# Kernel optimization log

Measured on AMD Instinct MI355X. Metric: run time of the kernel, lower is better.

## Reference

```python
import jax, jax.numpy as jnp
import numpy as np

C = 0.01          # curvature
SQRT_C = C ** 0.5 # 0.1
R = 16            # number of diagonal blocks = out_features / block_size
BS = 256          # block_size
D = R * BS        # 4096


def _artanh(x):
    # Matches torch Artanh: clamp input, grad is 1/(1-xc^2) (straight-through clamp)
    xc = jnp.clip(x, -1.0 + 1e-5, 1.0 - 1e-5)
    xc = x + jax.lax.stop_gradient(xc - x)
    return 0.5 * (jnp.log(1.0 + xc) - jnp.log(1.0 - xc))


def _tanh(x, clamp=15.0):
    return jnp.tanh(jnp.clip(x, -clamp, clamp))


def _norm(x):
    return jnp.linalg.norm(x, axis=-1, keepdims=True)


def _forward(x, weights):
    # expmap0 (poincare ball)
    u_norm = jnp.maximum(_norm(x), 1e-5)
    h = _tanh(SQRT_C * u_norm) * x / (SQRT_C * u_norm)
    # fix_filt = output_hyperbolic.data  -> detach
    h = jax.lax.stop_gradient(h)

    # mobius_matvec with block-diagonal weight; equivalent batched block matmul:
    # mx = h @ block_diag(W_1..W_r).T  ==  per-block h_r @ W_r.T
    xb = h.reshape(h.shape[:-1] + (R, BS))            # [..., r, bs]
    mx = jnp.einsum('...rk,rjk->...rj', xb, weights)  # [..., r, bs]
    mx = mx.reshape(h.shape)

    x_norm = jnp.maximum(_norm(h), 1e-5)
    mx_norm = _norm(mx)
    res_c = _tanh(mx_norm / x_norm * _artanh(SQRT_C * x_norm)) * mx / (mx_norm * SQRT_C)
    cond = jnp.all(mx == 0, axis=-1, keepdims=True)
    res = jnp.where(cond, jnp.zeros((), dtype=res_c.dtype), res_c)

    # _project onto the ball
    nrm = jnp.maximum(_norm(res), 1e-5)
    maxnorm = (1.0 - 1e-3) / SQRT_C
    res = jnp.where(nrm > maxnorm, res / nrm * maxnorm, res)

    # logmap0 (poincare ball)
    y_norm = jnp.maximum(_norm(res), 1e-5)
    return res / y_norm / SQRT_C * _artanh(SQRT_C * y_norm)


def setup_inputs() -> dict:
    key = jax.random.key(0)
    k1, k2 = jax.random.split(key)
    x = jax.random.normal(k1, (4, 2048, D), dtype=jnp.float32)
    # params: init is stack of identity blocks; add small noise so math is non-trivial
    eye = jnp.broadcast_to(jnp.eye(BS, dtype=jnp.float32), (R, BS, BS))
    weights = eye + 0.02 * jax.random.normal(k2, (R, BS, BS), dtype=jnp.float32)
    return {"x": x, "weights": weights}


def reference(x, weights):
    return _forward(x, weights)
```

## Files before the change

### kernel.cpp

```cpp
#include <hip/hip_runtime.h>


typedef __attribute__((ext_vector_type(8))) short short8;
typedef __attribute__((ext_vector_type(4))) float f32x4;

__device__ __forceinline__ ushort f2bf(float f) {
  uint u = __float_as_uint(f);
  return (ushort)((u + 0x7fffu + ((u >> 16) & 1u)) >> 16);
}

__global__ __launch_bounds__(256) void wrepack_kernel(const float* __restrict__ w,
                                                      ushort* __restrict__ wb2) {
  int idx = blockIdx.x * blockDim.x + threadIdx.x;
  int lane = idx & 63;
  int nt = (idx >> 6) & 15;
  int kf = (idx >> 10) & 7;
  int blk = idx >> 13;
  int g = lane >> 4, q = lane & 15;
  const float* src = w + ((size_t)blk << 16) + (size_t)(nt * 16 + q) * 256 + kf * 32 + g * 8;
  float4 v0 = *reinterpret_cast<const float4*>(src);
  float4 v1 = *reinterpret_cast<const float4*>(src + 4);
  ushort o[8] = {f2bf(v0.x), f2bf(v0.y), f2bf(v0.z), f2bf(v0.w),
                 f2bf(v1.x), f2bf(v1.y), f2bf(v1.z), f2bf(v1.w)};
  uint4 p;
  p.x = (uint)o[0] | ((uint)o[1] << 16);
  p.y = (uint)o[2] | ((uint)o[3] << 16);
  p.z = (uint)o[4] | ((uint)o[5] << 16);
  p.w = (uint)o[6] | ((uint)o[7] << 16);
  reinterpret_cast<uint4*>(wb2)[idx] = p;
}

__global__ __launch_bounds__(1024, 4) void hyp_kernel(const float* __restrict__ x,
                                                      const ushort* __restrict__ wb2,
                                                      float* __restrict__ out) {
  __shared__ ushort xs[16 * 4096];
  __shared__ float ssxp[16];
  __shared__ float sspm[16][16];
  __shared__ float gam[16];

  const int tid = threadIdx.x;
  const int w = tid >> 6;
  const int lane = tid & 63;
  const int g = lane >> 4;
  const int q = lane & 15;
  const size_t rowbase = (size_t)blockIdx.x * 16;

  {
    const float4* xr = reinterpret_cast<const float4*>(x + (rowbase + w) * 4096);
    char* xrow = reinterpret_cast<char*>(xs);
    const uint sw = (uint)(w & 7) << 4;
    float ss = 0.f;
#pragma unroll
    for (int chunk = 0; chunk < 16; ++chunk) {
      float4 v = xr[chunk * 64 + lane];
      ss += v.x * v.x + v.y * v.y + v.z * v.z + v.w * v.w;
      uint2 p;
      p.x = (uint)f2bf(v.x) | ((uint)f2bf(v.y) << 16);
      p.y = (uint)f2bf(v.z) | ((uint)f2bf(v.w) << 16);
      uint byte = ((uint)(w * 8192 + (chunk * 64 + lane) * 8)) ^ sw;
      *reinterpret_cast<uint2*>(xrow + byte) = p;
    }
#pragma unroll
    for (int m = 32; m; m >>= 1) ss += __shfl_xor(ss, m, 64);
    if (lane == 0) ssxp[w] = ss;
  }
  __syncthreads();

  f32x4 acc[16];
#pragma unroll
  for (int nt = 0; nt < 16; ++nt) acc[nt] = (f32x4){0.f, 0.f, 0.f, 0.f};

  for (int kf = 0; kf < 8; ++kf) {
    uint abyte = ((uint)(q * 8192 + w * 512 + kf * 64 + g * 16)) ^ ((uint)(q & 7) << 4);
    short8 afr = *reinterpret_cast<const short8*>(reinterpret_cast<const char*>(xs) + abyte);
    const ushort* bkf = wb2 + ((((size_t)w * 8 + kf) * 16) << 9) + (lane << 3);
#pragma unroll
    for (int nt = 0; nt < 16; ++nt) {
      short8 bfr = *reinterpret_cast<const short8*>(bkf + (nt << 9));
      acc[nt] = __builtin_amdgcn_mfma_f32_16x16x32_bf16(afr, bfr, acc[nt], 0, 0, 0);
    }
  }

  {
    float s0 = 0.f, s1 = 0.f, s2a = 0.f, s3 = 0.f;
#pragma unroll
    for (int nt = 0; nt < 16; ++nt) {
      f32x4 a = acc[nt];
      s0 += a[0] * a[0];
      s1 += a[1] * a[1];
      s2a += a[2] * a[2];
      s3 += a[3] * a[3];
    }
#pragma unroll
    for (int m = 1; m < 16; m <<= 1) {
      s0 += __shfl_xor(s0, m, 64);
      s1 += __shfl_xor(s1, m, 64);
      s2a += __shfl_xor(s2a, m, 64);
      s3 += __shfl_xor(s3, m, 64);
    }
    if (q == 0) {
      sspm[w][g * 4 + 0] = s0;
      sspm[w][g * 4 + 1] = s1;
      sspm[w][g * 4 + 2] = s2a;
      sspm[w][g * 4 + 3] = s3;
    }
  }
  __syncthreads();

  if (tid < 16) {
    float s2 = 0.f;
#pragma unroll
    for (int ww = 0; ww < 16; ++ww) s2 += sspm[ww][tid];
    const float xnorm = sqrtf(ssxp[tid]);
    const float un = fmaxf(xnorm, 1e-5f);
    const float a0 = 0.1f * un;
    const float th = tanhf(fminf(a0, 15.f));
    const float c = th / a0;
    const float hn = th * (xnorm / a0);
    const float xn = fmaxf(hn, 1e-5f);
    const float sp = sqrtf(s2);
    float gt = 0.f;
    if (sp > 0.f) {
      const float s = c * sp;
      const float xc = fminf(0.1f * xn, 1.f - 1e-5f);
      const float at = 0.5f * logf((1.f + xc) / (1.f - xc));
      const float t = (s / xn) * at;
      const float tn = tanhf(fminf(t, 15.f));
      const float alpha = tn / (0.1f * s);
      const float rn = tn * 10.f;
      const float nrm = fmaxf(rn, 1e-5f);
      const float proj = (nrm > 9.99f) ? (9.99f / nrm) : 1.f;
      const float yn = fmaxf(rn * proj, 1e-5f);
      const float yc = fminf(0.1f * yn, 1.f - 1e-5f);
      const float at2 = 0.5f * logf((1.f + yc) / (1.f - yc));
      gt = c * alpha * proj * (at2 / (0.1f * yn));
    }
    gam[tid] = gt;
  }
  __syncthreads();

  char* ob = reinterpret_cast<char*>(xs);
  float gr[4];
#pragma unroll
  for (int j = 0; j < 4; ++j) gr[j] = gam[g * 4 + j];

#pragma unroll
  for (int p = 0; p < 2; ++p) {
    if ((w >> 3) == p) {
      const int wl = w & 7;
#pragma unroll
      for (int nt = 0; nt < 16; ++nt) {
#pragma unroll
        for (int j = 0; j < 4; ++j) {
          const int row = g * 4 + j;
          const int col = wl * 256 + nt * 16 + q;
          uint byte = ((uint)(row * 8192 + col * 4)) ^ ((uint)(row & 7) << 4);
          *reinterpret_cast<float*>(ob + byte) = gr[j] * acc[nt][j];
        }
      }
    }
    __syncthreads();
    {
      const char* rb = ob + w * 8192;
      const uint sw = (uint)(w & 7) << 4;
      float* op = out + (rowbase + w) * 4096 + p * 2048;
#pragma unroll
      for (int i = 0; i < 8; ++i) {
        uint byte = ((uint)(lane * 16 + i * 1024)) ^ sw;
        f32x4 v = *reinterpret_cast<const f32x4*>(rb + byte);
        *reinterpret_cast<f32x4*>(op + lane * 4 + i * 256) = v;
      }
    }
    __syncthreads();
  }
}

__global__ __launch_bounds__(1024, 4) void hyp_fallback(const float* __restrict__ x,
                                                        const float* __restrict__ wf,
                                                        float* __restrict__ out) {
  __shared__ float ssxp[16][16];
  __shared__ float sspm[16][16];
  __shared__ float gam[16];
  const int tid = threadIdx.x;
  const int w = tid >> 6;
  const int lane = tid & 63;
  const int g = lane >> 4, q = lane & 15;
  const size_t rowbase = (size_t)blockIdx.x * 16;
  f32x4 acc[16];
#pragma unroll
  for (int nt = 0; nt < 16; ++nt) acc[nt] = (f32x4){0.f, 0.f, 0.f, 0.f};
  const float* xbase = x + (rowbase + q) * 4096 + w * 256 + g * 8;
  const float* wfbase = wf + ((size_t)w << 16) + (size_t)q * 256 + g * 8;
  float ssx = 0.f;
  for (int kf = 0; kf < 8; ++kf) {
    const float* xp = xbase + kf * 32;
    float4 v0 = *reinterpret_cast<const float4*>(xp);
    float4 v1 = *reinterpret_cast<const float4*>(xp + 4);
    ssx += v0.x * v0.x + v0.y * v0.y + v0.z * v0.z + v0.w * v0.w +
           v1.x * v1.x + v1.y * v1.y + v1.z * v1.z + v1.w * v1.w;
    short8 afr;
    afr[0] = (short)f2bf(v0.x); afr[1] = (short)f2bf(v0.y);
    afr[2] = (short)f2bf(v0.z); afr[3] = (short)f2bf(v0.w);
    afr[4] = (short)f2bf(v1.x); afr[5] = (short)f2bf(v1.y);
    afr[6] = (short)f2bf(v1.z); afr[7] = (short)f2bf(v1.w);
#pragma unroll
    for (int nt = 0; nt < 16; ++nt) {
      const float* wp = wfbase + nt * 4096 + kf * 32;
      float4 w0 = *reinterpret_cast<const float4*>(wp);
      float4 w1 = *reinterpret_cast<const float4*>(wp + 4);
      short8 bfr;
      bfr[0] = (short)f2bf(w0.x); bfr[1] = (short)f2bf(w0.y);
      bfr[2] = (short)f2bf(w0.z); bfr[3] = (short)f2bf(w0.w);
      bfr[4] = (short)f2bf(w1.x); bfr[5] = (short)f2bf(w1.y);
      bfr[6] = (short)f2bf(w1.z); bfr[7] = (short)f2bf(w1.w);
      acc[nt] = __builtin_amdgcn_mfma_f32_16x16x32_bf16(afr, bfr, acc[nt], 0, 0, 0);
    }
  }
  ssx += __shfl_xor(ssx, 16, 64);
  ssx += __shfl_xor(ssx, 32, 64);
  if (g == 0) ssxp[w][q] = ssx;
  float s0 = 0.f, s1 = 0.f, s2a = 0.f, s3 = 0.f;
#pragma unroll
  for (int nt = 0; nt < 16; ++nt) {
    f32x4 a = acc[nt];
    s0 += a[0] * a[0]; s1 += a[1] * a[1]; s2a += a[2] * a[2]; s3 += a[3] * a[3];
  }
#pragma unroll
  for (int m = 1; m < 16; m <<= 1) {
    s0 += __shfl_xor(s0, m, 64); s1 += __shfl_xor(s1, m, 64);
    s2a += __shfl_xor(s2a, m, 64); s3 += __shfl_xor(s3, m, 64);
  }
  if (q == 0) {
    sspm[w][g * 4 + 0] = s0; sspm[w][g * 4 + 1] = s1;
    sspm[w][g * 4 + 2] = s2a; sspm[w][g * 4 + 3] = s3;
  }
  __syncthreads();
  if (tid < 16) {
    float sx = 0.f, s2 = 0.f;
#pragma unroll
    for (int ww = 0; ww < 16; ++ww) { sx += ssxp[ww][tid]; s2 += sspm[ww][tid]; }
    const float xnorm = sqrtf(sx);
    const float un = fmaxf(xnorm, 1e-5f);
    const float a0 = 0.1f * un;
    const float th = tanhf(fminf(a0, 15.f));
    const float c = th / a0;
    const float hn = th * (xnorm / a0);
    const float xn = fmaxf(hn, 1e-5f);
    const float sp = sqrtf(s2);
    float gt = 0.f;
    if (sp > 0.f) {
      const float s = c * sp;
      const float xc = fminf(0.1f * xn, 1.f - 1e-5f);
      const float at = 0.5f * logf((1.f + xc) / (1.f - xc));
      const float t = (s / xn) * at;
      const float tn = tanhf(fminf(t, 15.f));
      const float alpha = tn / (0.1f * s);
      const float rn = tn * 10.f;
      const float nrm = fmaxf(rn, 1e-5f);
      const float proj = (nrm > 9.99f) ? (9.99f / nrm) : 1.f;
      const float yn = fmaxf(rn * proj, 1e-5f);
      const float yc = fminf(0.1f * yn, 1.f - 1e-5f);
      const float at2 = 0.5f * logf((1.f + yc) / (1.f - yc));
      gt = c * alpha * proj * (at2 / (0.1f * yn));
    }
    gam[tid] = gt;
  }
  __syncthreads();
  float gr[4];
#pragma unroll
  for (int j = 0; j < 4; ++j) gr[j] = gam[g * 4 + j];
  float* orow = out + rowbase * 4096 + w * 256;
#pragma unroll
  for (int nt = 0; nt < 16; ++nt) {
    const int col = nt * 16 + q;
    f32x4 a = acc[nt];
#pragma unroll
    for (int j = 0; j < 4; ++j) orow[(size_t)(g * 4 + j) * 4096 + col] = gr[j] * a[j];
  }
}

extern "C" void kernel_launch(void* const* d_in, const int* in_sizes, int n_in,
                              void* d_out, int out_size, void* d_ws, size_t ws_size,
                              hipStream_t stream) {
  const float* x = (const float*)d_in[0];
  const float* w = (const float*)d_in[1];
  float* out = (float*)d_out;

  const size_t wb_bytes = (size_t)16 * 8 * 16 * 64 * 8 * sizeof(ushort);
  if (ws_size >= wb_bytes) {
    ushort* wb2 = (ushort*)d_ws;
    wrepack_kernel<<<512, 256, 0, stream>>>(w, wb2);
    hyp_kernel<<<512, 1024, 0, stream>>>(x, wb2, out);
  } else {
    hyp_fallback<<<512, 1024, 0, stream>>>(x, w, out);
  }
}
```

Measured before the change: 116.1 us.

## Split into two-pass block-stationary GEMM with per-row gamma kernel

Replaces the single fused kernel with a weight-stationary scheme. Each workgroup holds one diagonal block's bf16 weights in registers and streams 256 rows. A first pass computes partial squared norms, a small kernel computes the per-row gamma, and a second pass recomputes the GEMM and writes the scaled output. This removes repeated global weight loads per row tile, at the cost of reading x twice and redoing the matmul. The old fp32 fallback path is dropped, so nothing runs when the workspace is smaller than the weight buffer.

```diff
diff --git a/kernel.cpp b/kernel.cpp
--- a/kernel.cpp
+++ b/kernel.cpp
@@ -7,6 +7,34 @@
 __device__ __forceinline__ ushort f2bf(float f) {
   uint u = __float_as_uint(f);
   return (ushort)((u + 0x7fffu + ((u >> 16) & 1u)) >> 16);
+}
+
+__device__ __forceinline__ float gamma_of(float sx, float s2) {
+  const float xnorm = sqrtf(sx);
+  const float un = fmaxf(xnorm, 1e-5f);
+  const float a0 = 0.1f * un;
+  const float th = tanhf(fminf(a0, 15.f));
+  const float c = th / a0;
+  const float hn = th * (xnorm / a0);
+  const float xn = fmaxf(hn, 1e-5f);
+  const float sp = sqrtf(s2);
+  float gt = 0.f;
+  if (sp > 0.f) {
+    const float s = c * sp;
+    const float xc = fminf(0.1f * xn, 1.f - 1e-5f);
+    const float at = 0.5f * logf((1.f + xc) / (1.f - xc));
+    const float t = (s / xn) * at;
+    const float tn = tanhf(fminf(t, 15.f));
+    const float alpha = tn / (0.1f * s);
+    const float rn = tn * 10.f;
+    const float nrm = fmaxf(rn, 1e-5f);
+    const float proj = (nrm > 9.99f) ? (9.99f / nrm) : 1.f;
+    const float yn = fmaxf(rn * proj, 1e-5f);
+    const float yc = fminf(0.1f * yn, 1.f - 1e-5f);
+    const float at2 = 0.5f * logf((1.f + yc) / (1.f - yc));
+    gt = c * alpha * proj * (at2 / (0.1f * yn));
+  }
+  return gt;
 }
 
 __global__ __launch_bounds__(256) void wrepack_kernel(const float* __restrict__ w,
@@ -20,31 +48,130 @@
   const float* src = w + ((size_t)blk << 16) + (size_t)(nt * 16 + q) * 256 + kf * 32 + g * 8;
   float4 v0 = *reinterpret_cast<const float4*>(src);
   float4 v1 = *reinterpret_cast<const float4*>(src + 4);
-  ushort o[8] = {f2bf(v0.x), f2bf(v0.y), f2bf(v0.z), f2bf(v0.w),
-                 f2bf(v1.x), f2bf(v1.y), f2bf(v1.z), f2bf(v1.w)};
   uint4 p;
-  p.x = (uint)o[0] | ((uint)o[1] << 16);
-  p.y = (uint)o[2] | ((uint)o[3] << 16);
-  p.z = (uint)o[4] | ((uint)o[5] << 16);
-  p.w = (uint)o[6] | ((uint)o[7] << 16);
+  p.x = (uint)f2bf(v0.x) | ((uint)f2bf(v0.y) << 16);
+  p.y = (uint)f2bf(v0.z) | ((uint)f2bf(v0.w) << 16);
+  p.z = (uint)f2bf(v1.x) | ((uint)f2bf(v1.y) << 16);
+  p.w = (uint)f2bf(v1.z) | ((uint)f2bf(v1.w) << 16);
   reinterpret_cast<uint4*>(wb2)[idx] = p;
 }
 
-__global__ __launch_bounds__(1024, 4) void hyp_kernel(const float* __restrict__ x,
-                                                      const ushort* __restrict__ wb2,
-                                                      float* __restrict__ out) {
-  __shared__ ushort xs[16 * 4096];
-  __shared__ float ssxp[16];
-  __shared__ float sspm[16][16];
-  __shared__ float gam[16];
+template <bool APPLY>
+__global__ __launch_bounds__(256, 2) void gemm_phase(const float* __restrict__ x,
+                                                     const ushort* __restrict__ wb2,
+                                                     float* __restrict__ ssxP,
+                                                     float* __restrict__ sspP,
+                                                     const float* __restrict__ gam,
+                                                     float* __restrict__ out) {
+  __shared__ ushort As[128 * 256];
+  __shared__ float sspw[4][128];
+  __shared__ float gl[128];
 
   const int tid = threadIdx.x;
   const int w = tid >> 6;
   const int lane = tid & 63;
   const int g = lane >> 4;
   const int q = lane & 15;
+  const int b = blockIdx.x & 15;
+  const int sg = blockIdx.x >> 4;
+
+  short8 barr[4][8];
+#pragma unroll
+  for (int i = 0; i < 4; ++i)
+#pragma unroll
+    for (int kf = 0; kf < 8; ++kf)
+      barr[i][kf] = *reinterpret_cast<const short8*>(
+          wb2 + ((((size_t)b * 8 + kf) * 16 + (w * 4 + i)) << 9) + (lane << 3));
+
+  for (int ss = 0; ss < 2; ++ss) {
+    const size_t rowbase = (size_t)sg * 256 + (size_t)ss * 128;
+
+    __syncthreads();
+    for (int r = 0; r < 32; ++r) {
+      const int lrow = w * 32 + r;
+      const float4 v = *reinterpret_cast<const float4*>(
+          x + (rowbase + lrow) * 4096 + b * 256 + lane * 4);
+      if (!APPLY) {
+        float ssq = v.x * v.x + v.y * v.y + v.z * v.z + v.w * v.w;
+#pragma unroll
+        for (int m = 32; m; m >>= 1) ssq += __shfl_xor(ssq, m, 64);
+        if (lane == 0) ssxP[b * 8192 + rowbase + lrow] = ssq;
+      }
+      uint2 p;
+      p.x = (uint)f2bf(v.x) | ((uint)f2bf(v.y) << 16);
+      p.y = (uint)f2bf(v.z) | ((uint)f2bf(v.w) << 16);
+      uint byte = ((uint)(lrow * 512 + lane * 8)) ^ ((uint)(lrow & 7) << 4);
+      *reinterpret_cast<uint2*>(reinterpret_cast<char*>(As) + byte) = p;
+    }
+    if (APPLY && tid < 128) gl[tid] = gam[rowbase + tid];
+    __syncthreads();
+
+    for (int rt = 0; rt < 8; ++rt) {
+      f32x4 acc[4];
+#pragma unroll
+      for (int i = 0; i < 4; ++i) acc[i] = (f32x4){0.f, 0.f, 0.f, 0.f};
+#pragma unroll
+      for (int kf = 0; kf < 8; ++kf) {
+        uint abyte = ((uint)((rt * 16 + q) * 512 + kf * 64 + g * 16)) ^ ((uint)(q & 7) << 4);
+        short8 afr = *reinterpret_cast<const short8*>(reinterpret_cast<const char*>(As) + abyte);
+#pragma unroll
+        for (int i = 0; i < 4; ++i)
+          acc[i] = __builtin_amdgcn_mfma_f32_16x16x32_bf16(afr, barr[i][kf], acc[i], 0, 0, 0);
+      }
+      if (!APPLY) {
+#pragma unroll
+        for (int j = 0; j < 4; ++j) {
+          float t = 0.f;
+#pragma unroll
+          for (int i = 0; i < 4; ++i) t += acc[i][j] * acc[i][j];
+#pragma unroll
+          for (int m = 1; m < 16; m <<= 1) t += __shfl_xor(t, m, 64);
+          if (q == 0) sspw[w][rt * 16 + g * 4 + j] = t;
+        }
+      } else {
+#pragma unroll
+        for (int i = 0; i < 4; ++i) {
+          float* op = out + (rowbase + rt * 16 + g * 4) * 4096 + b * 256 + (w * 4 + i) * 16 + q;
+#pragma unroll
+          for (int j = 0; j < 4; ++j) op[(size_t)j * 4096] = gl[rt * 16 + g * 4 + j] * acc[i][j];
+        }
+      }
+    }
+
+    if (!APPLY) {
+      __syncthreads();
+      if (tid < 128)
+        sspP[b * 8192 + rowbase + tid] =
+            sspw[0][tid] + sspw[1][tid] + sspw[2][tid] + sspw[3][tid];
+    }
+  }
+}
+
+__global__ __launch_bounds__(256) void gamma_kernel(const float* __restrict__ ssxP,
+                                                    const float* __restrict__ sspP,
+                                                    float* __restrict__ gam) {
+  const int row = blockIdx.x * 256 + threadIdx.x;
+  float sx = 0.f, s2 = 0.f;
+#pragma unroll
+  for (int bb = 0; bb < 16; ++bb) {
+    sx += ssxP[bb * 8192 + row];
+    s2 += sspP[bb * 8192 + row];
+  }
+  gam[row] = gamma_of(sx, s2);
+}
+
+__global__ __launch_bounds__(1024, 4) void hyp_fused(const float* __restrict__ x,
+                                                     const ushort* __restrict__ wb2,
+                                                     float* __restrict__ out) {
+  __shared__ ushort xs[16 * 4096];
+  __shared__ float ssxp[16];
+  __shared__ float sspm[16][16];
+  __shared__ float gamv[16];
+  const int tid = threadIdx.x;
+  const int w = tid >> 6;
+  const int lane = tid & 63;
+  const int g = lane >> 4, q = lane & 15;
   const size_t rowbase = (size_t)blockIdx.x * 16;
-
   {
     const float4* xr = reinterpret_cast<const float4*>(x + (rowbase + w) * 4096);
     char* xrow = reinterpret_cast<char*>(xs);
@@ -65,11 +192,9 @@
     if (lane == 0) ssxp[w] = ss;
   }
   __syncthreads();
-
   f32x4 acc[16];
 #pragma unroll
   for (int nt = 0; nt < 16; ++nt) acc[nt] = (f32x4){0.f, 0.f, 0.f, 0.f};
-
   for (int kf = 0; kf < 8; ++kf) {
     uint abyte = ((uint)(q * 8192 + w * 512 + kf * 64 + g * 16)) ^ ((uint)(q & 7) << 4);
     short8 afr = *reinterpret_cast<const short8*>(reinterpret_cast<const char*>(xs) + abyte);
@@ -80,195 +205,34 @@
       acc[nt] = __builtin_amdgcn_mfma_f32_16x16x32_bf16(afr, bfr, acc[nt], 0, 0, 0);
     }
   }
-
   {
     float s0 = 0.f, s1 = 0.f, s2a = 0.f, s3 = 0.f;
 #pragma unroll
     for (int nt = 0; nt < 16; ++nt) {
       f32x4 a = acc[nt];
-      s0 += a[0] * a[0];
-      s1 += a[1] * a[1];
-      s2a += a[2] * a[2];
-      s3 += a[3] * a[3];
+      s0 += a[0] * a[0]; s1 += a[1] * a[1]; s2a += a[2] * a[2]; s3 += a[3] * a[3];
     }
 #pragma unroll
     for (int m = 1; m < 16; m <<= 1) {
-      s0 += __shfl_xor(s0, m, 64);
-      s1 += __shfl_xor(s1, m, 64);
-      s2a += __shfl_xor(s2a, m, 64);
-      s3 += __shfl_xor(s3, m, 64);
+      s0 += __shfl_xor(s0, m, 64); s1 += __shfl_xor(s1, m, 64);
+      s2a += __shfl_xor(s2a, m, 64); s3 += __shfl_xor(s3, m, 64);
     }
     if (q == 0) {
-      sspm[w][g * 4 + 0] = s0;
-      sspm[w][g * 4 + 1] = s1;
-      sspm[w][g * 4 + 2] = s2a;
-      sspm[w][g * 4 + 3] = s3;
+      sspm[w][g * 4 + 0] = s0; sspm[w][g * 4 + 1] = s1;
+      sspm[w][g * 4 + 2] = s2a; sspm[w][g * 4 + 3] = s3;
     }
   }
   __syncthreads();
-
   if (tid < 16) {
     float s2 = 0.f;
 #pragma unroll
     for (int ww = 0; ww < 16; ++ww) s2 += sspm[ww][tid];
-    const float xnorm = sqrtf(ssxp[tid]);
-    const float un = fmaxf(xnorm, 1e-5f);
-    const float a0 = 0.1f * un;
-    const float th = tanhf(fminf(a0, 15.f));
-    const float c = th / a0;
-    const float hn = th * (xnorm / a0);
-    const float xn = fmaxf(hn, 1e-5f);
-    const float sp = sqrtf(s2);
-    float gt = 0.f;
-    if (sp > 0.f) {
-      const float s = c * sp;
-      const float xc = fminf(0.1f * xn, 1.f - 1e-5f);
-      const float at = 0.5f * logf((1.f + xc) / (1.f - xc));
-      const float t = (s / xn) * at;
-      const float tn = tanhf(fminf(t, 15.f));
-      const float alpha = tn / (0.1f * s);
-      const float rn = tn * 10.f;
-      const float nrm = fmaxf(rn, 1e-5f);
-      const float proj = (nrm > 9.99f) ? (9.99f / nrm) : 1.f;
-      const float yn = fmaxf(rn * proj, 1e-5f);
-      const float yc = fminf(0.1f * yn, 1.f - 1e-5f);
-      const float at2 = 0.5f * logf((1.f + yc) / (1.f - yc));
-      gt = c * alpha * proj * (at2 / (0.1f * yn));
-    }
-    gam[tid] = gt;
-  }
-  __syncthreads();
-
-  char* ob = reinterpret_cast<char*>(xs);
-  float gr[4];
-#pragma unroll
-  for (int j = 0; j < 4; ++j) gr[j] = gam[g * 4 + j];
-
-#pragma unroll
-  for (int p = 0; p < 2; ++p) {
-    if ((w >> 3) == p) {
-      const int wl = w & 7;
-#pragma unroll
-      for (int nt = 0; nt < 16; ++nt) {
-#pragma unroll
-        for (int j = 0; j < 4; ++j) {
-          const int row = g * 4 + j;
-          const int col = wl * 256 + nt * 16 + q;
-          uint byte = ((uint)(row * 8192 + col * 4)) ^ ((uint)(row & 7) << 4);
-          *reinterpret_cast<float*>(ob + byte) = gr[j] * acc[nt][j];
-        }
-      }
-    }
-    __syncthreads();
-    {
-      const char* rb = ob + w * 8192;
-      const uint sw = (uint)(w & 7) << 4;
-      float* op = out + (rowbase + w) * 4096 + p * 2048;
-#pragma unroll
-      for (int i = 0; i < 8; ++i) {
-        uint byte = ((uint)(lane * 16 + i * 1024)) ^ sw;
-        f32x4 v = *reinterpret_cast<const f32x4*>(rb + byte);
-        *reinterpret_cast<f32x4*>(op + lane * 4 + i * 256) = v;
-      }
-    }
-    __syncthreads();
-  }
-}
-
-__global__ __launch_bounds__(1024, 4) void hyp_fallback(const float* __restrict__ x,
-                                                        const float* __restrict__ wf,
-                                                        float* __restrict__ out) {
-  __shared__ float ssxp[16][16];
-  __shared__ float sspm[16][16];
-  __shared__ float gam[16];
-  const int tid = threadIdx.x;
-  const int w = tid >> 6;
-  const int lane = tid & 63;
-  const int g = lane >> 4, q = lane & 15;
-  const size_t rowbase = (size_t)blockIdx.x * 16;
-  f32x4 acc[16];
-#pragma unroll
-  for (int nt = 0; nt < 16; ++nt) acc[nt] = (f32x4){0.f, 0.f, 0.f, 0.f};
-  const float* xbase = x + (rowbase + q) * 4096 + w * 256 + g * 8;
-  const float* wfbase = wf + ((size_t)w << 16) + (size_t)q * 256 + g * 8;
-  float ssx = 0.f;
-  for (int kf = 0; kf < 8; ++kf) {
-    const float* xp = xbase + kf * 32;
-    float4 v0 = *reinterpret_cast<const float4*>(xp);
-    float4 v1 = *reinterpret_cast<const float4*>(xp + 4);
-    ssx += v0.x * v0.x + v0.y * v0.y + v0.z * v0.z + v0.w * v0.w +
-           v1.x * v1.x + v1.y * v1.y + v1.z * v1.z + v1.w * v1.w;
-    short8 afr;
-    afr[0] = (short)f2bf(v0.x); afr[1] = (short)f2bf(v0.y);
-    afr[2] = (short)f2bf(v0.z); afr[3] = (short)f2bf(v0.w);
-    afr[4] = (short)f2bf(v1.x); afr[5] = (short)f2bf(v1.y);
-    afr[6] = (short)f2bf(v1.z); afr[7] = (short)f2bf(v1.w);
-#pragma unroll
-    for (int nt = 0; nt < 16; ++nt) {
-      const float* wp = wfbase + nt * 4096 + kf * 32;
-      float4 w0 = *reinterpret_cast<const float4*>(wp);
-      float4 w1 = *reinterpret_cast<const float4*>(wp + 4);
-      short8 bfr;
-      bfr[0] = (short)f2bf(w0.x); bfr[1] = (short)f2bf(w0.y);
-      bfr[2] = (short)f2bf(w0.z); bfr[3] = (short)f2bf(w0.w);
-      bfr[4] = (short)f2bf(w1.x); bfr[5] = (short)f2bf(w1.y);
-      bfr[6] = (short)f2bf(w1.z); bfr[7] = (short)f2bf(w1.w);
-      acc[nt] = __builtin_amdgcn_mfma_f32_16x16x32_bf16(afr, bfr, acc[nt], 0, 0, 0);
-    }
-  }
-  ssx += __shfl_xor(ssx, 16, 64);
-  ssx += __shfl_xor(ssx, 32, 64);
-  if (g == 0) ssxp[w][q] = ssx;
-  float s0 = 0.f, s1 = 0.f, s2a = 0.f, s3 = 0.f;
-#pragma unroll
-  for (int nt = 0; nt < 16; ++nt) {
-    f32x4 a = acc[nt];
-    s0 += a[0] * a[0]; s1 += a[1] * a[1]; s2a += a[2] * a[2]; s3 += a[3] * a[3];
-  }
-#pragma unroll
-  for (int m = 1; m < 16; m <<= 1) {
-    s0 += __shfl_xor(s0, m, 64); s1 += __shfl_xor(s1, m, 64);
-    s2a += __shfl_xor(s2a, m, 64); s3 += __shfl_xor(s3, m, 64);
-  }
-  if (q == 0) {
-    sspm[w][g * 4 + 0] = s0; sspm[w][g * 4 + 1] = s1;
-    sspm[w][g * 4 + 2] = s2a; sspm[w][g * 4 + 3] = s3;
-  }
-  __syncthreads();
-  if (tid < 16) {
-    float sx = 0.f, s2 = 0.f;
-#pragma unroll
-    for (int ww = 0; ww < 16; ++ww) { sx += ssxp[ww][tid]; s2 += sspm[ww][tid]; }
-    const float xnorm = sqrtf(sx);
-    const float un = fmaxf(xnorm, 1e-5f);
-    const float a0 = 0.1f * un;
-    const float th = tanhf(fminf(a0, 15.f));
-    const float c = th / a0;
-    const float hn = th * (xnorm / a0);
-    const float xn = fmaxf(hn, 1e-5f);
-    const float sp = sqrtf(s2);
-    float gt = 0.f;
-    if (sp > 0.f) {
-      const float s = c * sp;
-      const float xc = fminf(0.1f * xn, 1.f - 1e-5f);
-      const float at = 0.5f * logf((1.f + xc) / (1.f - xc));
-      const float t = (s / xn) * at;
-      const float tn = tanhf(fminf(t, 15.f));
-      const float alpha = tn / (0.1f * s);
-      const float rn = tn * 10.f;
-      const float nrm = fmaxf(rn, 1e-5f);
-      const float proj = (nrm > 9.99f) ? (9.99f / nrm) : 1.f;
-      const float yn = fmaxf(rn * proj, 1e-5f);
-      const float yc = fminf(0.1f * yn, 1.f - 1e-5f);
-      const float at2 = 0.5f * logf((1.f + yc) / (1.f - yc));
-      gt = c * alpha * proj * (at2 / (0.1f * yn));
-    }
-    gam[tid] = gt;
+    gamv[tid] = gamma_of(ssxp[tid], s2);
   }
   __syncthreads();
   float gr[4];
 #pragma unroll
-  for (int j = 0; j < 4; ++j) gr[j] = gam[g * 4 + j];
+  for (int j = 0; j < 4; ++j) gr[j] = gamv[g * 4 + j];
   float* orow = out + rowbase * 4096 + w * 256;
 #pragma unroll
   for (int nt = 0; nt < 16; ++nt) {
@@ -286,12 +250,24 @@
   const float* w = (const float*)d_in[1];
   float* out = (float*)d_out;
 
-  const size_t wb_bytes = (size_t)16 * 8 * 16 * 64 * 8 * sizeof(ushort);
-  if (ws_size >= wb_bytes) {
+  const size_t WB = (size_t)2 << 20;
+  const size_t SSX_OFF = WB;
+  const size_t SSP_OFF = WB + ((size_t)512 << 10);
+  const size_t GAM_OFF = WB + ((size_t)1 << 20);
+  const size_t NEED = GAM_OFF + (size_t)8192 * 4;
+
+  if (ws_size >= NEED) {
+    ushort* wb2 = (ushort*)d_ws;
+    float* ssxP = (float*)((char*)d_ws + SSX_OFF);
+    float* sspP = (float*)((char*)d_ws + SSP_OFF);
+    float* gamv = (float*)((char*)d_ws + GAM_OFF);
+    wrepack_kernel<<<512, 256, 0, stream>>>(w, wb2);
+    gemm_phase<false><<<512, 256, 0, stream>>>(x, wb2, ssxP, sspP, nullptr, nullptr);
+    gamma_kernel<<<32, 256, 0, stream>>>(ssxP, sspP, gamv);
+    gemm_phase<true><<<512, 256, 0, stream>>>(x, wb2, nullptr, nullptr, gamv, out);
+  } else if (ws_size >= WB) {
     ushort* wb2 = (ushort*)d_ws;
     wrepack_kernel<<<512, 256, 0, stream>>>(w, wb2);
-    hyp_kernel<<<512, 1024, 0, stream>>>(x, wb2, out);
-  } else {
-    hyp_fallback<<<512, 1024, 0, stream>>>(x, w, out);
-  }
-}
+    hyp_fused<<<512, 1024, 0, stream>>>(x, wb2, out);
+  }
+}
```

New measurement: 170.4 us. 46.8% more time.
